# Optimization experiments

Hardware: AMD Instinct MI355X
Metric: run time of the kernel (lower is better)

The kernel has to match this reference:

```python
import jax, jax.numpy as jnp
import numpy as np

P = 0.9  # CLOP swap probability (init kwarg)


def _index_permute(key, n_element, dim):
    """Faithful port of CLOPLayer._index_permute: sequential conditional
    neighbor swaps over a flat index array, expressed as a lax.scan.
    Swap choices r in {0..4} with probs (1-p/2, p/8, p/8, p/8, p/8);
    r maps to offset {0, +1, -1, +dim, -dim}; swap only if r!=0 and
    0 < idx < n_element (strict >0, matching the original code)."""
    probs = jnp.array([1.0 - P / 2, P / 8, P / 8, P / 8, P / 8], dtype=jnp.float32)
    # loop runs i over abs(range(-n+1, n)) -> 2n-1 steps
    iters = jnp.abs(jnp.arange(-n_element + 1, n_element, dtype=jnp.int32))
    rs = jax.random.choice(key, 5, shape=(iters.shape[0],), p=probs)
    offsets = jnp.array([0, 1, -1, dim, -dim], dtype=jnp.int32)

    def step(perm, inp):
        i, r = inp
        idx = i + offsets[r]
        do = (r != 0) & (idx > 0) & (idx < n_element)
        idx_c = jnp.clip(idx, 0, n_element - 1)
        a = perm[i]
        b = perm[idx_c]
        # conditional swap; when do is False both writes restore originals
        perm = perm.at[i].set(jnp.where(do, b, a))
        perm = perm.at[idx_c].set(jnp.where(do, a, b))
        return perm, None

    perm0 = jnp.arange(n_element, dtype=jnp.int32)
    perm, _ = jax.lax.scan(step, perm0, (iters, rs))
    return perm


def setup_inputs() -> dict:
    key = jax.random.key(0)
    x = jax.random.normal(key, (512, 9, 84, 84), dtype=jnp.float32)
    return {"x": x}


def reference(x):
    B, C, H, W = x.shape
    n = H * W  # n_element of x[0,0]; dim = int(sqrt(n)) == H for square images
    perm = _index_permute(jax.random.key(42), n, H)
    flat = x.reshape(B, C, n)
    # torch.gather(flat, 2, idx) with idx broadcast over (B, C)
    res = jnp.take(flat, perm, axis=2)
    return res.reshape(x.shape)
```

## Files before the change

kernel.cpp:

```cpp
#include <hip/hip_runtime.h>

#define N_ELEM   7056
#define DIM      84
#define M_STEPS  14111
#define N_ROWS   4608
#define NCHUNK   384
#define KSTEPS   37
#define WINW     208
#define TPB      256
#define NJV      1764

#define TRACE_BLOCKS 28
#define GROUPS   16
#define CPG      (NCHUNK / GROUPS)
#define ROWS_PB  4

__device__ __forceinline__ void threefry2x32(unsigned k0, unsigned k1,
                                             unsigned x0, unsigned x1,
                                             unsigned &o0, unsigned &o1) {
  const unsigned ks0 = k0, ks1 = k1, ks2 = k0 ^ k1 ^ 0x1BD11BDAu;
  x0 += ks0; x1 += ks1;
#define ROTL(x, r) (((x) << (r)) | ((x) >> (32 - (r))))
#define RND(r) { x0 += x1; x1 = ROTL(x1, r); x1 ^= x0; }
  RND(13) RND(15) RND(26) RND(6)
  x0 += ks1; x1 += ks2 + 1u;
  RND(17) RND(29) RND(16) RND(24)
  x0 += ks2; x1 += ks0 + 2u;
  RND(13) RND(15) RND(26) RND(6)
  x0 += ks0; x1 += ks1 + 3u;
  RND(17) RND(29) RND(16) RND(24)
  x0 += ks1; x1 += ks2 + 4u;
  RND(13) RND(15) RND(26) RND(6)
  x0 += ks2; x1 += ks0 + 5u;
  o0 = x0; o1 = x1;
#undef RND
#undef ROTL
}

__device__ __forceinline__ int r_from_bits(unsigned bits) {
  const float p8 = 0.1125f;
  const float q0 = 0.55f;
  const float q1 = q0 + p8;
  const float q2 = q1 + p8;
  const float q3 = q2 + p8;
  const float q4 = q3 + p8;
  float u  = __uint_as_float((bits >> 9) | 0x3F800000u) - 1.0f;
  float rv = q4 * (1.0f - u);
  return (int)(q0 < rv) + (int)(q1 < rv) + (int)(q2 < rv) + (int)(q3 < rv);
}

__device__ __forceinline__ void chunk_bounds(int c, int &t0, int &t1, int &lo, int &hi) {
  t0 = c * KSTEPS; if (t0 > M_STEPS) t0 = M_STEPS;
  t1 = t0 + KSTEPS; if (t1 > M_STEPS) t1 = M_STEPS;
  int a0 = t0 - (N_ELEM - 1);       if (a0 < 0) a0 = -a0;
  int a1 = (t1 - 1) - (N_ELEM - 1); if (a1 < 0) a1 = -a1;
  int imax = a0 > a1 ? a0 : a1;
  int imin;
  if (t0 <= N_ELEM - 1 && t1 - 1 >= N_ELEM - 1) imin = 0;
  else imin = a0 < a1 ? a0 : a1;
  lo = imin - DIM; if (lo < 0) lo = 0;
  hi = imax + DIM; if (hi > N_ELEM - 1) hi = N_ELEM - 1;
}

__global__ __launch_bounds__(TPB) void chunk_kernel(unsigned* __restrict__ winG) {
  __shared__ __align__(16) unsigned short w[WINW];
  __shared__ unsigned char rs[KSTEPS + 3];

  const int c = blockIdx.x, tid = threadIdx.x;
  int t0, t1, lo, hi; chunk_bounds(c, t0, t1, lo, hi);
  const int nt = t1 - t0;

  if (tid < WINW) w[tid] = (unsigned short)(lo + tid);
  if (tid < nt) {
    unsigned y0, y1;
    threefry2x32(0u, 42u, 0u, (unsigned)(t0 + tid), y0, y1);
    rs[tid] = (unsigned char)r_from_bits(y0 ^ y1);
  }
  __syncthreads();

  if (tid == 0) {
    for (int k = 0; k < nt; ++k) {
      int t = t0 + k;
      int i = t - (N_ELEM - 1); if (i < 0) i = -i;
      int r = rs[k];
      int off = (r == 1) ? 1 : (r == 2) ? -1 : (r == 3) ? DIM : (r == 4) ? -DIM : 0;
      int idx = i + off;
      bool doit = (r != 0) && (idx > 0) && (idx < N_ELEM);
      int je = doit ? idx : i;
      unsigned short a = w[i  - lo];
      unsigned short b = w[je - lo];
      w[i  - lo] = b;
      w[je - lo] = a;
    }
  }
  __syncthreads();

  const uint4* w4 = (const uint4*)w;
  if (tid < WINW * 2 / 16) ((uint4*)winG)[c * (WINW * 2 / 16) + tid] = w4[tid];
}

__global__ __launch_bounds__(TPB) void partial_trace_kernel(const unsigned* __restrict__ winG,
                                                            unsigned short* __restrict__ Pg) {
  __shared__ __align__(16) unsigned short w[CPG * WINW];
  const int tid = threadIdx.x;
  const int g  = blockIdx.x / TRACE_BLOCKS;
  const int sb = blockIdx.x % TRACE_BLOCKS;
  const int U4_PER_WIN = WINW * 2 / 16;

  uint4* w4 = (uint4*)w;
  const uint4* g4 = (const uint4*)winG + (size_t)(g * CPG) * U4_PER_WIN;
  for (int k = tid; k < CPG * U4_PER_WIN; k += TPB) w4[k] = g4[k];
  __syncthreads();

  if (tid < 252) {
    int y = sb * 252 + tid;
    for (int c = CPG - 1; c >= 0; --c) {
      int t0, t1, lo, hi; chunk_bounds(g * CPG + c, t0, t1, lo, hi);
      unsigned e = (unsigned)(y - lo);
      if (e <= (unsigned)(hi - lo)) y = (int)w[c * WINW + e];
    }
    Pg[g * N_ELEM + sb * 252 + tid] = (unsigned short)y;
  }
}

__global__ __launch_bounds__(TPB) void compose_kernel(const unsigned short* __restrict__ Pg,
                                                      int* __restrict__ permG) {
  const int tid = threadIdx.x;
  if (tid >= 252) return;
  const int j = blockIdx.x * 252 + tid;
  int y = j;
#pragma unroll
  for (int g = GROUPS - 1; g >= 0; --g) y = (int)Pg[g * N_ELEM + y];
  permG[j] = y;
}

__global__ __launch_bounds__(TPB) void gather_kernel(const float* __restrict__ x,
                                                     const int* __restrict__ perm,
                                                     float* __restrict__ out) {
  __shared__ __align__(16) float row[N_ELEM];
  const int tid = threadIdx.x;
  const int r0 = blockIdx.x * ROWS_PB;

  int4 p[7];
  const int4* p4 = (const int4*)perm;
#pragma unroll
  for (int k = 0; k < 7; ++k) {
    int v = tid + k * TPB;
    if (v < NJV) p[k] = p4[v];
  }

  for (int rr = 0; rr < ROWS_PB; ++rr) {
    const int r = r0 + rr;
    const float4* xr4 = (const float4*)(x + (size_t)r * N_ELEM);
    float4* row4 = (float4*)row;
#pragma unroll
    for (int k = 0; k < 7; ++k) {
      int v = tid + k * TPB;
      if (v < NJV) row4[v] = xr4[v];
    }
    __syncthreads();

    float4* or4 = (float4*)(out + (size_t)r * N_ELEM);
#pragma unroll
    for (int k = 0; k < 7; ++k) {
      int v = tid + k * TPB;
      if (v < NJV) {
        int4 pp = p[k];
        float4 o;
        o.x = row[pp.x]; o.y = row[pp.y]; o.z = row[pp.z]; o.w = row[pp.w];
        or4[v] = o;
      }
    }
    __syncthreads();
  }
}

extern "C" void kernel_launch(void* const* d_in, const int* in_sizes, int n_in,
                              void* d_out, int out_size, void* d_ws, size_t ws_size,
                              hipStream_t stream) {
  const float* x = (const float*)d_in[0];
  float* out = (float*)d_out;

  unsigned* winG = (unsigned*)d_ws;
  unsigned short* Pg = (unsigned short*)((char*)d_ws + (size_t)NCHUNK * WINW * 2);
  int* perm = (int*)((char*)d_ws + (size_t)NCHUNK * WINW * 2
                                 + (size_t)GROUPS * N_ELEM * 2);

  chunk_kernel<<<NCHUNK, TPB, 0, stream>>>(winG);
  partial_trace_kernel<<<GROUPS * TRACE_BLOCKS, TPB, 0, stream>>>(winG, Pg);
  compose_kernel<<<TRACE_BLOCKS, TPB, 0, stream>>>(Pg, perm);
  gather_kernel<<<N_ROWS / ROWS_PB, TPB, 0, stream>>>(x, perm, out);
}
```

Before: 253.3 us.

## Fuse chunk and trace kernels, prefetch next row, use nontemporal stores in gather

Merges the per-chunk swap simulation into the partial-trace kernel so each trace block recomputes its group's chunk windows in shared memory. This removes one launch and the global round trip of window data, at the cost of redundant RNG and swap work across the 28 blocks per group. The gather kernel now prefetches the next row into registers while it permutes the current one, uses nontemporal stores for the output, and halves rows per block with an occupancy hint in launch bounds.

```diff
diff --git a/kernel.cpp b/kernel.cpp
--- a/kernel.cpp
+++ b/kernel.cpp
@@ -13,7 +13,9 @@
 #define TRACE_BLOCKS 28
 #define GROUPS   16
 #define CPG      (NCHUNK / GROUPS)
-#define ROWS_PB  4
+#define ROWS_PB  2
+
+typedef float fvec4 __attribute__((ext_vector_type(4)));
 
 __device__ __forceinline__ void threefry2x32(unsigned k0, unsigned k1,
                                              unsigned x0, unsigned x1,
@@ -62,54 +64,49 @@
   hi = imax + DIM; if (hi > N_ELEM - 1) hi = N_ELEM - 1;
 }
 
-__global__ __launch_bounds__(TPB) void chunk_kernel(unsigned* __restrict__ winG) {
-  __shared__ __align__(16) unsigned short w[WINW];
-  __shared__ unsigned char rs[KSTEPS + 3];
-
-  const int c = blockIdx.x, tid = threadIdx.x;
-  int t0, t1, lo, hi; chunk_bounds(c, t0, t1, lo, hi);
-  const int nt = t1 - t0;
-
-  if (tid < WINW) w[tid] = (unsigned short)(lo + tid);
-  if (tid < nt) {
+__global__ __launch_bounds__(TPB) void permbuild_kernel(unsigned short* __restrict__ Pg) {
+  __shared__ __align__(16) unsigned short w[CPG * WINW];
+  __shared__ unsigned char rs[CPG * KSTEPS];
+  const int tid = threadIdx.x;
+  const int g  = blockIdx.x / TRACE_BLOCKS;
+  const int sb = blockIdx.x % TRACE_BLOCKS;
+
+  for (int idx = tid; idx < CPG * WINW; idx += TPB) {
+    int c = idx / WINW;
+    int j = idx - c * WINW;
+    int t0, t1, lo, hi; chunk_bounds(g * CPG + c, t0, t1, lo, hi);
+    w[idx] = (unsigned short)(lo + j);
+  }
+  for (int q = tid; q < CPG * KSTEPS; q += TPB) {
+    int c = q / KSTEPS;
+    int k = q - c * KSTEPS;
+    int t = (g * CPG + c) * KSTEPS + k;
     unsigned y0, y1;
-    threefry2x32(0u, 42u, 0u, (unsigned)(t0 + tid), y0, y1);
-    rs[tid] = (unsigned char)r_from_bits(y0 ^ y1);
+    threefry2x32(0u, 42u, 0u, (unsigned)t, y0, y1);
+    rs[q] = (unsigned char)r_from_bits(y0 ^ y1);
   }
   __syncthreads();
 
-  if (tid == 0) {
+  if (tid < CPG) {
+    const int c = tid;
+    int t0, t1, lo, hi; chunk_bounds(g * CPG + c, t0, t1, lo, hi);
+    const int nt = t1 - t0;
+    unsigned short* wc = &w[c * WINW];
+    const unsigned char* rc = &rs[c * KSTEPS];
     for (int k = 0; k < nt; ++k) {
       int t = t0 + k;
       int i = t - (N_ELEM - 1); if (i < 0) i = -i;
-      int r = rs[k];
+      int r = rc[k];
       int off = (r == 1) ? 1 : (r == 2) ? -1 : (r == 3) ? DIM : (r == 4) ? -DIM : 0;
       int idx = i + off;
       bool doit = (r != 0) && (idx > 0) && (idx < N_ELEM);
       int je = doit ? idx : i;
-      unsigned short a = w[i  - lo];
-      unsigned short b = w[je - lo];
-      w[i  - lo] = b;
-      w[je - lo] = a;
-    }
-  }
-  __syncthreads();
-
-  const uint4* w4 = (const uint4*)w;
-  if (tid < WINW * 2 / 16) ((uint4*)winG)[c * (WINW * 2 / 16) + tid] = w4[tid];
-}
-
-__global__ __launch_bounds__(TPB) void partial_trace_kernel(const unsigned* __restrict__ winG,
-                                                            unsigned short* __restrict__ Pg) {
-  __shared__ __align__(16) unsigned short w[CPG * WINW];
-  const int tid = threadIdx.x;
-  const int g  = blockIdx.x / TRACE_BLOCKS;
-  const int sb = blockIdx.x % TRACE_BLOCKS;
-  const int U4_PER_WIN = WINW * 2 / 16;
-
-  uint4* w4 = (uint4*)w;
-  const uint4* g4 = (const uint4*)winG + (size_t)(g * CPG) * U4_PER_WIN;
-  for (int k = tid; k < CPG * U4_PER_WIN; k += TPB) w4[k] = g4[k];
+      unsigned short a = wc[i  - lo];
+      unsigned short b = wc[je - lo];
+      wc[i  - lo] = b;
+      wc[je - lo] = a;
+    }
+  }
   __syncthreads();
 
   if (tid < 252) {
@@ -134,12 +131,13 @@
   permG[j] = y;
 }
 
-__global__ __launch_bounds__(TPB) void gather_kernel(const float* __restrict__ x,
-                                                     const int* __restrict__ perm,
-                                                     float* __restrict__ out) {
+__global__ __launch_bounds__(TPB, 5) void gather_kernel(const float* __restrict__ x,
+                                                        const int* __restrict__ perm,
+                                                        float* __restrict__ out) {
   __shared__ __align__(16) float row[N_ELEM];
   const int tid = threadIdx.x;
   const int r0 = blockIdx.x * ROWS_PB;
+  float4* row4 = (float4*)row;
 
   int4 p[7];
   const int4* p4 = (const int4*)perm;
@@ -149,26 +147,42 @@
     if (v < NJV) p[k] = p4[v];
   }
 
-  for (int rr = 0; rr < ROWS_PB; ++rr) {
-    const int r = r0 + rr;
-    const float4* xr4 = (const float4*)(x + (size_t)r * N_ELEM);
-    float4* row4 = (float4*)row;
+  float4 buf[7];
+  {
+    const float4* xr4 = (const float4*)(x + (size_t)r0 * N_ELEM);
 #pragma unroll
     for (int k = 0; k < 7; ++k) {
       int v = tid + k * TPB;
-      if (v < NJV) row4[v] = xr4[v];
+      if (v < NJV) buf[k] = xr4[v];
+    }
+  }
+
+  for (int rr = 0; rr < ROWS_PB; ++rr) {
+#pragma unroll
+    for (int k = 0; k < 7; ++k) {
+      int v = tid + k * TPB;
+      if (v < NJV) row4[v] = buf[k];
     }
     __syncthreads();
 
-    float4* or4 = (float4*)(out + (size_t)r * N_ELEM);
+    if (rr + 1 < ROWS_PB) {
+      const float4* xn4 = (const float4*)(x + (size_t)(r0 + rr + 1) * N_ELEM);
+#pragma unroll
+      for (int k = 0; k < 7; ++k) {
+        int v = tid + k * TPB;
+        if (v < NJV) buf[k] = xn4[v];
+      }
+    }
+
+    fvec4* or4 = (fvec4*)(out + (size_t)(r0 + rr) * N_ELEM);
 #pragma unroll
     for (int k = 0; k < 7; ++k) {
       int v = tid + k * TPB;
       if (v < NJV) {
         int4 pp = p[k];
-        float4 o;
+        fvec4 o;
         o.x = row[pp.x]; o.y = row[pp.y]; o.z = row[pp.z]; o.w = row[pp.w];
-        or4[v] = o;
+        __builtin_nontemporal_store(o, &or4[v]);
       }
     }
     __syncthreads();
@@ -181,13 +195,10 @@
   const float* x = (const float*)d_in[0];
   float* out = (float*)d_out;
 
-  unsigned* winG = (unsigned*)d_ws;
-  unsigned short* Pg = (unsigned short*)((char*)d_ws + (size_t)NCHUNK * WINW * 2);
-  int* perm = (int*)((char*)d_ws + (size_t)NCHUNK * WINW * 2
-                                 + (size_t)GROUPS * N_ELEM * 2);
-
-  chunk_kernel<<<NCHUNK, TPB, 0, stream>>>(winG);
-  partial_trace_kernel<<<GROUPS * TRACE_BLOCKS, TPB, 0, stream>>>(winG, Pg);
+  unsigned short* Pg = (unsigned short*)d_ws;
+  int* perm = (int*)((char*)d_ws + (size_t)GROUPS * N_ELEM * 2);
+
+  permbuild_kernel<<<GROUPS * TRACE_BLOCKS, TPB, 0, stream>>>(Pg);
   compose_kernel<<<TRACE_BLOCKS, TPB, 0, stream>>>(Pg, perm);
   gather_kernel<<<N_ROWS / ROWS_PB, TPB, 0, stream>>>(x, perm, out);
 }
```

Measured after the change: 275.4 us. 8.7% more time.
